# Performance work log

Hardware: AMD Instinct MI355X
Metric: run time of the kernel (lower is better)

The kernel has to match this reference:

```python
import jax, jax.numpy as jnp
import numpy as np

NUM_CLASSES = 20
K = 3
STRIDE = 32
IMG = 2048


def setup_inputs() -> dict:
    key = jax.random.key(0)
    k1, k2, k3, k4, k5, k6, k7 = jax.random.split(key, 7)
    B, Cin, H, W = 2, 1024, 64, 64
    N = 1000
    feats = jax.random.normal(k1, (B, Cin, H, W), jnp.float32)
    s = 1.0 / np.sqrt(Cin).astype(np.float32)
    w_cls = jax.random.normal(k2, ((NUM_CLASSES + 1) * K * K, Cin), jnp.float32) * s
    b_cls = jax.random.normal(k3, ((NUM_CLASSES + 1) * K * K,), jnp.float32) * 0.01
    w_reg = jax.random.normal(k4, (4 * K * K, Cin), jnp.float32) * s
    b_reg = jax.random.normal(k5, (4 * K * K,), jnp.float32) * 0.01
    # proposals in image pixel coords (x1, y1, x2, y2), guaranteed non-empty
    xy1 = jax.random.randint(k6, (B, N, 2), 0, IMG - 64)
    wh = jax.random.randint(k7, (B, N, 2), STRIDE, 512)
    xy2 = jnp.minimum(xy1 + wh, IMG)
    proposals = jnp.concatenate([xy1, xy2], axis=-1).astype(jnp.int32)
    return {"features": feats, "w_cls": w_cls, "b_cls": b_cls,
            "w_reg": w_reg, "b_reg": b_reg, "proposals": proposals}


def _psroi(scores, proposals, groups):
    """Faithful to the source: adaptive_avg_pool2d bin (0,0) per channel,
    then sum over the K*K channel groups (stride-::K*K indexing in torch)."""
    B, C, H, W = scores.shape
    N = proposals.shape[1]
    p = proposals.astype(jnp.float32) / STRIDE
    x1 = jnp.floor(p[..., 0]).astype(jnp.int32)  # [B,N]
    y1 = jnp.floor(p[..., 1]).astype(jnp.int32)
    x2 = jnp.ceil(p[..., 2]).astype(jnp.int32)
    y2 = jnp.ceil(p[..., 3]).astype(jnp.int32)
    # adaptive_avg_pool2d bin (0,0): rows [0, ceil(h/K)), cols [0, ceil(w/K)) of the crop
    hb = (y2 - y1 + K - 1) // K
    wb = (x2 - x1 + K - 1) // K
    r = jnp.arange(H)
    c = jnp.arange(W)
    rmask = (r[None, None, :] >= y1[..., None]) & (r[None, None, :] < (y1 + hb)[..., None])  # [B,N,H]
    cmask = (c[None, None, :] >= x1[..., None]) & (c[None, None, :] < (x1 + wb)[..., None])  # [B,N,W]
    mask = (rmask[..., :, None] & cmask[..., None, :]).astype(scores.dtype)  # [B,N,H,W]
    denom = (hb * wb).astype(scores.dtype)
    pooled = jnp.einsum('bohw,bnhw->bno', scores, mask) / denom[..., None]  # bin(0,0) avg, all channels
    # channel index = cls_group * K*K + g ; torch ::K*K picks (g, spatial_bin 0) then sums over g
    return pooled.reshape(B, N, groups, K * K).sum(-1)


def reference(features, w_cls, b_cls, w_reg, b_reg, proposals):
    cls_scores = jnp.einsum('bchw,oc->bohw', features, w_cls) + b_cls[None, :, None, None]
    reg_scores = jnp.einsum('bchw,oc->bohw', features, w_reg) + b_reg[None, :, None, None]
    cls_out = _psroi(cls_scores, proposals, NUM_CLASSES + 1)  # [B,N,21]
    reg_out = _psroi(reg_scores, proposals, 4)                # [B,N,4]
    return (cls_out, reg_out)
```

## Files before the change

kernel.cpp:

```cpp
#include <hip/hip_runtime.h>


#define HW 4096
#define NG 25
#define CIN 1024
#define B 2
#define NPROP 1000
#define NCH 2
#define CK (CIN / NCH)
#define NSL 16
#define CS (CK / NSL)
#define MHW (B * NG * HW)

__global__ __launch_bounds__(1024)
void rfcn_projf(const float* __restrict__ feats,
                const float* __restrict__ w_cls,
                const float* __restrict__ w_reg,
                float* __restrict__ part) {
    const int t = threadIdx.x;
    const int chunk = blockIdx.y;
    const int b = blockIdx.z;
    __shared__ float wlds[NG * CK];
    __shared__ float red[NSL * NG * 64];

    for (int idx = t; idx < NG * CK; idx += 1024) {
        const int g = idx / CK;
        const int c = idx - g * CK;
        const int gc = chunk * CK + c;
        float s = 0.f;
        if (g < 21) {
            #pragma unroll
            for (int k = 0; k < 9; ++k) s += w_cls[(size_t)(g * 9 + k) * CIN + gc];
        } else {
            const int gr = g - 21;
            #pragma unroll
            for (int k = 0; k < 9; ++k) s += w_reg[(size_t)(gr * 9 + k) * CIN + gc];
        }
        wlds[idx] = s;
    }
    __syncthreads();

    const int p = t & 63;
    const int sl = __builtin_amdgcn_readfirstlane(t >> 6);
    const int pix0 = blockIdx.x * 64;
    const int c0 = chunk * CK + sl * CS;

    const float* __restrict__ f = feats + ((size_t)b * CIN + c0) * HW + pix0 + p;
    const float4* __restrict__ w4 = (const float4*)(wlds + sl * CS);

    float acc[NG];
    #pragma unroll
    for (int g = 0; g < NG; ++g) acc[g] = 0.f;

    float fv[CS];
    #pragma unroll
    for (int j = 0; j < CS; ++j) fv[j] = f[(size_t)j * HW];

    #pragma unroll
    for (int g = 0; g < NG; ++g) {
        float a = 0.f;
        #pragma unroll
        for (int q = 0; q < CS / 4; ++q) {
            const float4 w = w4[(size_t)g * (CK / 4) + q];
            a += fv[4 * q]     * w.x;
            a += fv[4 * q + 1] * w.y;
            a += fv[4 * q + 2] * w.z;
            a += fv[4 * q + 3] * w.w;
        }
        acc[g] = a;
    }

    #pragma unroll
    for (int g = 0; g < NG; ++g) red[(sl * NG + g) * 64 + p] = acc[g];
    __syncthreads();

    float* __restrict__ o = part + ((size_t)(chunk * B + b) * NG) * HW + pix0;
    for (int idx = t; idx < NG * 64; idx += 1024) {
        const int g = idx >> 6, pp = idx & 63;
        float s = 0.f;
        #pragma unroll
        for (int ss = 0; ss < NSL; ++ss) s += red[(ss * NG + g) * 64 + pp];
        o[(size_t)g * HW + pp] = s;
    }
}

__global__ __launch_bounds__(1024)
void rfcn_ig(const float* __restrict__ part,
             const int* __restrict__ props,
             const float* __restrict__ b_cls,
             const float* __restrict__ b_reg,
             float* __restrict__ out) {
    const int m = blockIdx.x;
    const int t = threadIdx.x;
    const int lane = t & 63;
    const int wave = t >> 6;
    const int b = m / NG;
    const int g = m - b * NG;
    __shared__ float tile[64 * 65];

    float bias = 0.f;
    if (g < 21) {
        #pragma unroll
        for (int k = 0; k < 9; ++k) bias += b_cls[g * 9 + k];
    } else {
        #pragma unroll
        for (int k = 0; k < 9; ++k) bias += b_reg[(g - 21) * 9 + k];
    }

    #pragma unroll
    for (int i = 0; i < 4; ++i) {
        const int idx = i * 1024 + t;
        const float v = part[(size_t)m * HW + idx]
                      + part[(size_t)(B * NG + m) * HW + idx];
        tile[(idx >> 6) * 65 + (idx & 63)] = v;
    }
    __syncthreads();

    #pragma unroll
    for (int i = 0; i < 4; ++i) {
        const int row = wave * 4 + i;
        float v = tile[row * 65 + lane];
        #pragma unroll
        for (int d = 1; d < 64; d <<= 1) {
            float u = __shfl_up(v, (unsigned)d, 64);
            if (lane >= d) v += u;
        }
        tile[row * 65 + lane] = v;
    }
    __syncthreads();

    #pragma unroll
    for (int i = 0; i < 4; ++i) {
        const int col = wave * 4 + i;
        float v = tile[lane * 65 + col];
        #pragma unroll
        for (int d = 1; d < 64; d <<= 1) {
            float u = __shfl_up(v, (unsigned)d, 64);
            if (lane >= d) v += u;
        }
        tile[lane * 65 + col] = v;
    }
    __syncthreads();

    const int n = t;
    if (n < NPROP) {
        const int4 pr = ((const int4*)props)[b * NPROP + n];
        const int x1 = pr.x >> 5;
        const int y1 = pr.y >> 5;
        const int x2 = (pr.z + 31) >> 5;
        const int y2 = (pr.w + 31) >> 5;
        const int wb = (x2 - x1 + 2) / 3;
        const int hb = (y2 - y1 + 2) / 3;
        const int c2 = x1 + wb - 1;
        const int r2 = y1 + hb - 1;

        float s = tile[r2 * 65 + c2];
        if (x1 > 0)           s -= tile[r2 * 65 + (x1 - 1)];
        if (y1 > 0)           s -= tile[(y1 - 1) * 65 + c2];
        if (x1 > 0 && y1 > 0) s += tile[(y1 - 1) * 65 + (x1 - 1)];
        const float v = bias + s / (float)(hb * wb);
        if (g < 21)
            out[(size_t)(b * NPROP + n) * 21 + g] = v;
        else
            out[(size_t)(B * NPROP * 21) + (size_t)(b * NPROP + n) * 4 + (g - 21)] = v;
    }
}

extern "C" void kernel_launch(void* const* d_in, const int* in_sizes, int n_in,
                              void* d_out, int out_size, void* d_ws, size_t ws_size,
                              hipStream_t stream) {
    const float* feats = (const float*)d_in[0];
    const float* w_cls = (const float*)d_in[1];
    const float* b_cls = (const float*)d_in[2];
    const float* w_reg = (const float*)d_in[3];
    const float* b_reg = (const float*)d_in[4];
    const int*   props = (const int*)d_in[5];
    float* out = (float*)d_out;
    float* ws  = (float*)d_ws;

    float* part = ws;

    rfcn_projf<<<dim3(HW / 64, NCH, B), 1024, 0, stream>>>(
        feats, w_cls, w_reg, part);
    rfcn_ig<<<B * NG, 1024, 0, stream>>>(part, props, b_cls, b_reg, out);
}
```

Baseline: 31.06 us.

## Split channels into four chunks with 512-thread blocks and two-stage LDS reduction

Channel split count goes from 2 to 4 and slices per block from 16 to 8, so the projection kernel launches twice as many 512-thread blocks, each covering 256 channels. Per-thread channel work (CS=32) stays the same, while per-block LDS shrinks: weights drop to 25x256 floats and the reduction buffer is halved by having half the waves add their results into the other half's slots. The aim is more resident blocks per CU and less weight-staging time per block. In exchange, the gather kernel must read and sum four partial buffers instead of two, and the workspace holds twice as many partials.

```diff
diff --git a/kernel.cpp b/kernel.cpp
--- a/kernel.cpp
+++ b/kernel.cpp
@@ -6,13 +6,13 @@
 #define CIN 1024
 #define B 2
 #define NPROP 1000
-#define NCH 2
+#define NCH 4
 #define CK (CIN / NCH)
-#define NSL 16
+#define NSL 8
 #define CS (CK / NSL)
 #define MHW (B * NG * HW)
 
-__global__ __launch_bounds__(1024)
+__global__ __launch_bounds__(512)
 void rfcn_projf(const float* __restrict__ feats,
                 const float* __restrict__ w_cls,
                 const float* __restrict__ w_reg,
@@ -21,11 +21,11 @@
     const int chunk = blockIdx.y;
     const int b = blockIdx.z;
     __shared__ float wlds[NG * CK];
-    __shared__ float red[NSL * NG * 64];
+    __shared__ float red[(NSL / 2) * NG * 64];
 
-    for (int idx = t; idx < NG * CK; idx += 1024) {
-        const int g = idx / CK;
-        const int c = idx - g * CK;
+    for (int idx = t; idx < NG * CK; idx += 512) {
+        const int g = idx >> 8;
+        const int c = idx & (CK - 1);
         const int gc = chunk * CK + c;
         float s = 0.f;
         if (g < 21) {
@@ -70,16 +70,22 @@
         acc[g] = a;
     }
 
-    #pragma unroll
-    for (int g = 0; g < NG; ++g) red[(sl * NG + g) * 64 + p] = acc[g];
+    if (sl >= 4) {
+        #pragma unroll
+        for (int g = 0; g < NG; ++g) red[((sl - 4) * NG + g) * 64 + p] = acc[g];
+    }
+    __syncthreads();
+    if (sl < 4) {
+        #pragma unroll
+        for (int g = 0; g < NG; ++g) red[(sl * NG + g) * 64 + p] += acc[g];
+    }
     __syncthreads();
 
     float* __restrict__ o = part + ((size_t)(chunk * B + b) * NG) * HW + pix0;
-    for (int idx = t; idx < NG * 64; idx += 1024) {
+    for (int idx = t; idx < NG * 64; idx += 512) {
         const int g = idx >> 6, pp = idx & 63;
-        float s = 0.f;
-        #pragma unroll
-        for (int ss = 0; ss < NSL; ++ss) s += red[(ss * NG + g) * 64 + pp];
+        float s = red[(0 * NG + g) * 64 + pp] + red[(1 * NG + g) * 64 + pp]
+                + red[(2 * NG + g) * 64 + pp] + red[(3 * NG + g) * 64 + pp];
         o[(size_t)g * HW + pp] = s;
     }
 }
@@ -110,9 +116,15 @@
     #pragma unroll
     for (int i = 0; i < 4; ++i) {
         const int idx = i * 1024 + t;
-        const float v = part[(size_t)m * HW + idx]
-                      + part[(size_t)(B * NG + m) * HW + idx];
-        tile[(idx >> 6) * 65 + (idx & 63)] = v;
+        float v[NCH];
+        #pragma unroll
+        for (int ch = 0; ch < NCH; ++ch)
+            v[ch] = part[(size_t)(ch * (B * NG) + m) * HW + idx];
+        #pragma unroll
+        for (int off = NCH / 2; off >= 1; off >>= 1)
+            #pragma unroll
+            for (int j = 0; j < off; ++j) v[j] += v[j + off];
+        tile[(idx >> 6) * 65 + (idx & 63)] = v[0];
     }
     __syncthreads();
 
@@ -180,7 +192,7 @@
 
     float* part = ws;
 
-    rfcn_projf<<<dim3(HW / 64, NCH, B), 1024, 0, stream>>>(
+    rfcn_projf<<<dim3(HW / 64, NCH, B), 512, 0, stream>>>(
         feats, w_cls, w_reg, part);
     rfcn_ig<<<B * NG, 1024, 0, stream>>>(part, props, b_cls, b_reg, out);
 }
```

Measured after the change: 31.67 us. About the same (+2.0%).
